# Kernel tuning notes

Hardware: AMD Instinct MI355X
Metric: run time of the kernel (lower is better)

Reference implementation:

```python
import jax, jax.numpy as jnp
import numpy as np


def setup_inputs() -> dict:
    key = jax.random.key(0)
    k1, k2 = jax.random.split(key)
    B, L1, L2, D = 8, 2048, 2048, 128
    seq_1 = jax.random.normal(k1, (B, L1, D), dtype=jnp.float32)
    seq_2 = jax.random.normal(k2, (B, L2, D), dtype=jnp.float32)
    return {"seq_1": seq_1, "seq_2": seq_2}


def reference(seq_1, seq_2):
    # e_ij: [B, L1, L2] cross-attention scores
    e_ij = jnp.einsum("bid,bjd->bij", seq_1, seq_2)
    # softmax over seq_2 positions (axis=2) to attend into seq_2
    w2 = jax.nn.softmax(e_ij, axis=2)
    # softmax over seq_1 positions (axis=1) to attend into seq_1
    w1 = jax.nn.softmax(e_ij, axis=1)
    seq_1_hat = jnp.einsum("bij,bjd->bid", w2, seq_2)  # [B, L1, D]
    seq_2_hat = jnp.einsum("bij,bid->bjd", w1, seq_1)  # [B, L2, D]
    return (seq_1_hat, seq_2_hat)
```

## Files before the change

kernel.cpp:

```cpp
#include <hip/hip_runtime.h>
#include <hip/hip_bf16.h>
#include <math.h>


#define LSEQ 2048
#define DIM  128
#define NBATCH 8
#define BM 128
#define BJ 128
#define NJT (LSEQ / BJ)
#define THR_DEFER 8.0f
#define PLANE (NBATCH * LSEQ * DIM)

typedef _Float16 halfT;
typedef halfT v8h  __attribute__((ext_vector_type(8)));
typedef float v16f __attribute__((ext_vector_type(16)));

__device__ __forceinline__ unsigned pk2u(float a, float b) {
    auto p = __builtin_amdgcn_cvt_pkrtz(a, b);
    return __builtin_bit_cast(unsigned, p);
}

__device__ __forceinline__ void gload16(const void* g, void* l) {
    __builtin_amdgcn_global_load_lds(
        (const __attribute__((address_space(1))) unsigned int*)g,
        (__attribute__((address_space(3))) unsigned int*)l, 16, 0, 0);
}

__device__ __forceinline__ v16f vz16() {
    v16f z;
    #pragma unroll
    for (int r = 0; r < 16; ++r) z[r] = 0.f;
    return z;
}

__global__ __launch_bounds__(256, 4)
void prepass_kernel(const float* __restrict__ S1, const float* __restrict__ S2,
                    short* __restrict__ ws)
{
    __shared__ short Th[DIM][66];
    const int lt = blockIdx.x;
    const int bb = blockIdx.y;
    const int tn = blockIdx.z;
    const float* src = (tn ? S2 : S1) + ((size_t)bb * LSEQ + (size_t)lt * 64) * DIM;
    short* hi = ws + (size_t)tn * 2 * PLANE + ((size_t)bb * LSEQ + (size_t)lt * 64) * DIM;
    short* tr = ws + (size_t)tn * 2 * PLANE + (size_t)PLANE
              + (size_t)bb * DIM * LSEQ + (size_t)lt * 64;
    const int tid = threadIdx.x;
    #pragma unroll
    for (int it = 0; it < 8; ++it) {
        int idx = tid + it * 256;
        int r = idx >> 5;
        int c = (idx & 31) * 4;
        float4 v = *(const float4*)(src + (size_t)r * DIM + c);
        halfT h0 = (halfT)v.x, h1 = (halfT)v.y, h2 = (halfT)v.z, h3 = (halfT)v.w;
        short b0 = __builtin_bit_cast(short, h0), b1 = __builtin_bit_cast(short, h1);
        short b2 = __builtin_bit_cast(short, h2), b3 = __builtin_bit_cast(short, h3);
        *(short4*)&hi[(size_t)r * DIM + c] = make_short4(b0, b1, b2, b3);
        Th[c + 0][r] = b0; Th[c + 1][r] = b1;
        Th[c + 2][r] = b2; Th[c + 3][r] = b3;
    }
    __syncthreads();
    #pragma unroll
    for (int it = 0; it < 16; ++it) {
        int idx = tid + it * 256;
        int d = idx >> 5;
        int c = (idx & 31) * 2;
        unsigned val = (unsigned)(unsigned short)Th[d][c]
                     | ((unsigned)(unsigned short)Th[d][c + 1] << 16);
        *(unsigned*)(tr + (size_t)d * LSEQ + c) = val;
    }
}

__global__ __launch_bounds__(1024, 1)
void xattn_main(const short* __restrict__ ws, float* __restrict__ out)
{
    __shared__ char pool[131072];
    __shared__ float maxp[4][4][32];
    __shared__ float sEx[4][4][32];

    const int tid  = threadIdx.x;
    const int lane = tid & 63;
    const int wave = tid >> 6;
    const int wA   = wave & 3;
    const int wB   = wave >> 2;
    const int li   = lane & 31;
    const int h    = lane >> 5;
    const int sl   = (li & 15) << 4;

    const int bx   = blockIdx.x;
    const int xcd  = bx & 7;
    const int slot = bx >> 3;
    const int g    = xcd * 2 + (slot >> 4);
    const int rt   = slot & 15;
    const int side = g >> 3;
    const int bb   = g & 7;

    const short* XHg = ws + (size_t)side * 2 * PLANE + ((size_t)bb * LSEQ + (size_t)rt * BM) * DIM;
    const short* YHg = ws + (size_t)(side ^ 1) * 2 * PLANE + (size_t)bb * LSEQ * DIM;
    const short* YTg = ws + (size_t)(side ^ 1) * 2 * PLANE + (size_t)PLANE + (size_t)bb * DIM * LSEQ;
    float* O = out + (size_t)side * PLANE + ((size_t)bb * LSEQ + (size_t)rt * BM) * DIM;

    v8h xv[8];
    {
        const short* xr = XHg + (size_t)(wA * 32 + li) * DIM + h * 8;
        #pragma unroll
        for (int ks = 0; ks < 8; ++ks)
            xv[ks] = *(const v8h*)(const void*)(xr + ks * 16);
    }

    float runm = -INFINITY, runs = 0.f;
    v16f o = vz16();

    const int ch0 = wave * 2;
    const int sr0 = ch0 * 4 + (lane >> 4);
    const int sr1 = (ch0 + 1) * 4 + (lane >> 4);
    const int sc0 = ((lane & 15) * 16) ^ ((sr0 & 15) << 4);
    const int sc1 = ((lane & 15) * 16) ^ ((sr1 & 15) << 4);

    auto STAGE_Y = [&](int jt) {
        gload16((const char*)YHg + ((size_t)(jt * BJ + sr0)) * 256 + sc0,
                pool + ch0 * 1024);
        gload16((const char*)YHg + ((size_t)(jt * BJ + sr1)) * 256 + sc1,
                pool + (ch0 + 1) * 1024);
    };
    auto STAGE_V = [&](int jt, int b) {
        gload16((const char*)YTg + (size_t)sr0 * (LSEQ * 2) + (size_t)jt * (BJ * 2) + sc0,
                pool + 32768 + b * 32768 + ch0 * 1024);
        gload16((const char*)YTg + (size_t)sr1 * (LSEQ * 2) + (size_t)jt * (BJ * 2) + sc1,
                pool + 32768 + b * 32768 + (ch0 + 1) * 1024);
    };

    STAGE_Y(0);
    STAGE_V(0, 0);
    asm volatile("s_waitcnt vmcnt(0)" ::: "memory");
    __syncthreads();

    const int yrow = wB * 32 + li;
    const int prow = wA * 32 + li;
    const int vrow = wB * 32 + li;
    char* PtB = pool + 98304;

    for (int jt = 0; jt < NJT; ++jt) {
        const int cur = jt & 1;

        v16f e = vz16();
        __builtin_amdgcn_s_setprio(1);
        #pragma unroll
        for (int ks = 0; ks < 8; ++ks) {
            v8h ya = *(const v8h*)(pool + yrow * 256 + ((ks * 32 + h * 16) ^ sl));
            e = __builtin_amdgcn_mfma_f32_32x32x16_f16(ya, xv[ks], e, 0, 0, 0);
        }
        __builtin_amdgcn_s_setprio(0);

        float a0 = fmaxf(fmaxf(e[0], e[1]),  fmaxf(e[2], e[3]));
        float a1 = fmaxf(fmaxf(e[4], e[5]),  fmaxf(e[6], e[7]));
        float a2 = fmaxf(fmaxf(e[8], e[9]),  fmaxf(e[10], e[11]));
        float a3 = fmaxf(fmaxf(e[12], e[13]), fmaxf(e[14], e[15]));
        float mt = fmaxf(fmaxf(a0, a1), fmaxf(a2, a3));
        mt = fmaxf(mt, __shfl_xor(mt, 32));
        if (lane < 32) maxp[wA][wB][lane] = mt;

        asm volatile("s_waitcnt lgkmcnt(0)" ::: "memory");
        __builtin_amdgcn_s_barrier();
        __builtin_amdgcn_sched_barrier(0);

        if (jt + 1 < NJT) {
            STAGE_Y(jt + 1);
            STAGE_V(jt + 1, cur ^ 1);
        }

        float m4 = fmaxf(fmaxf(maxp[wA][0][li], maxp[wA][1][li]),
                         fmaxf(maxp[wA][2][li], maxp[wA][3][li]));
        float f = 1.0f;
        if (m4 > runm + THR_DEFER) { f = __expf(runm - m4); runs *= f; runm = m4; }

        float s = 0.f;
        #pragma unroll
        for (int r = 0; r < 16; ++r) { e[r] = __expf(e[r] - runm); s += e[r]; }
        s += __shfl_xor(s, 32);
        runs += s;

        if (__any(f != 1.0f)) {
            #pragma unroll
            for (int r = 0; r < 16; ++r)
                o[r] *= __shfl(f, (r & 3) + 8 * (r >> 2) + 4 * h);
        }

        #pragma unroll
        for (int gq = 0; gq < 4; ++gq) {
            unsigned u0 = pk2u(e[gq * 4 + 0], e[gq * 4 + 1]);
            unsigned u1 = pk2u(e[gq * 4 + 2], e[gq * 4 + 3]);
            unsigned long long uu = (unsigned long long)u0 | ((unsigned long long)u1 << 32);
            const int gran = (wB * 4 + gq) ^ (li & 15);
            *(unsigned long long*)(PtB + prow * 256 + gran * 16 + h * 8) = uu;
        }

        asm volatile("s_waitcnt lgkmcnt(0)" ::: "memory");
        __builtin_amdgcn_s_barrier();
        __builtin_amdgcn_sched_barrier(0);

        const char* Vc = pool + 32768 + cur * 32768;
        __builtin_amdgcn_s_setprio(1);
        #pragma unroll
        for (int ks = 0; ks < 8; ++ks) {
            v8h pa = *(const v8h*)(PtB + prow * 256 + (((ks * 2 + h) ^ (li & 15)) << 4));
            v8h vb = *(const v8h*)(Vc + vrow * 256 + ((ks * 32 + h * 16) ^ sl));
            o = __builtin_amdgcn_mfma_f32_32x32x16_f16(pa, vb, o, 0, 0, 0);
        }
        __builtin_amdgcn_s_setprio(0);

        asm volatile("s_waitcnt vmcnt(0) lgkmcnt(0)" ::: "memory");
        __builtin_amdgcn_s_barrier();
        __builtin_amdgcn_sched_barrier(0);
    }

    if (lane < 32) sEx[wA][wB][lane] = runs;
    __syncthreads();
    const float inv = 1.0f / ((sEx[wA][0][li] + sEx[wA][1][li]) +
                              (sEx[wA][2][li] + sEx[wA][3][li]));
    #pragma unroll
    for (int r = 0; r < 16; ++r) {
        const int i = (r & 3) + 8 * (r >> 2) + 4 * h;
        const float fr = __shfl(inv, i);
        O[(size_t)(wA * 32 + i) * DIM + wB * 32 + li] = o[r] * fr;
    }
}

extern "C" void kernel_launch(void* const* d_in, const int* in_sizes, int n_in,
                              void* d_out, int out_size, void* d_ws, size_t ws_size,
                              hipStream_t stream) {
    const float* s1 = (const float*)d_in[0];
    const float* s2 = (const float*)d_in[1];
    float* out = (float*)d_out;
    short* ws = (short*)d_ws;
    prepass_kernel<<<dim3(LSEQ / 64, NBATCH, 2), 256, 0, stream>>>(s1, s2, ws);
    xattn_main<<<dim3(256), 1024, 0, stream>>>(ws, out);
}
```

Baseline: 68.81 us.

## Switch PV matmul to bf16, use a lagged row max, and restage Y/V buffers

The transposed value plane is now stored in bf16, and the probabilities are packed with v_cvt_pk_bf16_f32 so the PV MFMA runs in bf16. This widens the exponent range for the unnormalized weights. The softmax max now uses the previous tile's cross-wave maximum, which removes one block barrier per tile, and the rescale threshold drops to 4. Y is now double-buffered while V is single-buffered and staged after the PV step. Half of the X fragment is reloaded from global memory each tile to cut register pressure. The trade-offs are extra global loads, a risk of overflow from the lagged maximum, and serialization of the V load.

```diff
diff --git a/kernel.cpp b/kernel.cpp
--- a/kernel.cpp
+++ b/kernel.cpp
@@ -9,16 +9,24 @@
 #define BM 128
 #define BJ 128
 #define NJT (LSEQ / BJ)
-#define THR_DEFER 8.0f
+#define THR_DEFER 4.0f
 #define PLANE (NBATCH * LSEQ * DIM)
 
 typedef _Float16 halfT;
 typedef halfT v8h  __attribute__((ext_vector_type(8)));
+typedef short v8s  __attribute__((ext_vector_type(8)));
 typedef float v16f __attribute__((ext_vector_type(16)));
 
-__device__ __forceinline__ unsigned pk2u(float a, float b) {
-    auto p = __builtin_amdgcn_cvt_pkrtz(a, b);
-    return __builtin_bit_cast(unsigned, p);
+__device__ __forceinline__ unsigned pk2bf(float a, float b) {
+    unsigned r;
+    asm("v_cvt_pk_bf16_f32 %0, %1, %2" : "=v"(r) : "v"(a), "v"(b));
+    return r;
+}
+
+__device__ __forceinline__ short f2bf(float f) {
+    union { float f; unsigned u; } v; v.f = f;
+    unsigned r = (v.u + 0x7FFFu + ((v.u >> 16) & 1u)) >> 16;
+    return (short)r;
 }
 
 __device__ __forceinline__ void gload16(const void* g, void* l) {
@@ -54,11 +62,11 @@
         int c = (idx & 31) * 4;
         float4 v = *(const float4*)(src + (size_t)r * DIM + c);
         halfT h0 = (halfT)v.x, h1 = (halfT)v.y, h2 = (halfT)v.z, h3 = (halfT)v.w;
-        short b0 = __builtin_bit_cast(short, h0), b1 = __builtin_bit_cast(short, h1);
-        short b2 = __builtin_bit_cast(short, h2), b3 = __builtin_bit_cast(short, h3);
-        *(short4*)&hi[(size_t)r * DIM + c] = make_short4(b0, b1, b2, b3);
-        Th[c + 0][r] = b0; Th[c + 1][r] = b1;
-        Th[c + 2][r] = b2; Th[c + 3][r] = b3;
+        *(short4*)&hi[(size_t)r * DIM + c] = make_short4(
+            __builtin_bit_cast(short, h0), __builtin_bit_cast(short, h1),
+            __builtin_bit_cast(short, h2), __builtin_bit_cast(short, h3));
+        Th[c + 0][r] = f2bf(v.x); Th[c + 1][r] = f2bf(v.y);
+        Th[c + 2][r] = f2bf(v.z); Th[c + 3][r] = f2bf(v.w);
     }
     __syncthreads();
     #pragma unroll
@@ -76,7 +84,7 @@
 void xattn_main(const short* __restrict__ ws, float* __restrict__ out)
 {
     __shared__ char pool[131072];
-    __shared__ float maxp[4][4][32];
+    __shared__ float maxp[2][4][4][32];
     __shared__ float sEx[4][4][32];
 
     const int tid  = threadIdx.x;
@@ -101,15 +109,13 @@
     const short* YTg = ws + (size_t)(side ^ 1) * 2 * PLANE + (size_t)PLANE + (size_t)bb * DIM * LSEQ;
     float* O = out + (size_t)side * PLANE + ((size_t)bb * LSEQ + (size_t)rt * BM) * DIM;
 
-    v8h xv[8];
-    {
-        const short* xr = XHg + (size_t)(wA * 32 + li) * DIM + h * 8;
-        #pragma unroll
-        for (int ks = 0; ks < 8; ++ks)
-            xv[ks] = *(const v8h*)(const void*)(xr + ks * 16);
-    }
-
-    float runm = -INFINITY, runs = 0.f;
+    const short* xr = XHg + (size_t)(wA * 32 + li) * DIM + h * 8;
+    v8h xv[4];
+    #pragma unroll
+    for (int ks = 0; ks < 4; ++ks)
+        xv[ks] = *(const v8h*)(const void*)(xr + ks * 16);
+
+    float M = 0.f, runs = 0.f;
     v16f o = vz16();
 
     const int ch0 = wave * 2;
@@ -118,21 +124,21 @@
     const int sc0 = ((lane & 15) * 16) ^ ((sr0 & 15) << 4);
     const int sc1 = ((lane & 15) * 16) ^ ((sr1 & 15) << 4);
 
-    auto STAGE_Y = [&](int jt) {
+    auto STAGE_Y = [&](int jt, int b) {
         gload16((const char*)YHg + ((size_t)(jt * BJ + sr0)) * 256 + sc0,
-                pool + ch0 * 1024);
+                pool + b * 32768 + ch0 * 1024);
         gload16((const char*)YHg + ((size_t)(jt * BJ + sr1)) * 256 + sc1,
-                pool + (ch0 + 1) * 1024);
+                pool + b * 32768 + (ch0 + 1) * 1024);
     };
-    auto STAGE_V = [&](int jt, int b) {
+    auto STAGE_V = [&](int jt) {
         gload16((const char*)YTg + (size_t)sr0 * (LSEQ * 2) + (size_t)jt * (BJ * 2) + sc0,
-                pool + 32768 + b * 32768 + ch0 * 1024);
+                pool + 65536 + ch0 * 1024);
         gload16((const char*)YTg + (size_t)sr1 * (LSEQ * 2) + (size_t)jt * (BJ * 2) + sc1,
-                pool + 32768 + b * 32768 + (ch0 + 1) * 1024);
+                pool + 65536 + (ch0 + 1) * 1024);
     };
 
-    STAGE_Y(0);
-    STAGE_V(0, 0);
+    STAGE_Y(0, 0);
+    STAGE_V(0);
     asm volatile("s_waitcnt vmcnt(0)" ::: "memory");
     __syncthreads();
 
@@ -140,16 +146,28 @@
     const int prow = wA * 32 + li;
     const int vrow = wB * 32 + li;
     char* PtB = pool + 98304;
+    const char* Vc = pool + 65536;
 
     for (int jt = 0; jt < NJT; ++jt) {
         const int cur = jt & 1;
+        const char* Yc = pool + cur * 32768;
+
+        v8h xt[4];
+        #pragma unroll
+        for (int ks = 0; ks < 4; ++ks)
+            xt[ks] = *(const v8h*)(const void*)(xr + 64 + ks * 16);
 
         v16f e = vz16();
         __builtin_amdgcn_s_setprio(1);
         #pragma unroll
-        for (int ks = 0; ks < 8; ++ks) {
-            v8h ya = *(const v8h*)(pool + yrow * 256 + ((ks * 32 + h * 16) ^ sl));
+        for (int ks = 0; ks < 4; ++ks) {
+            v8h ya = *(const v8h*)(Yc + yrow * 256 + ((ks * 32 + h * 16) ^ sl));
             e = __builtin_amdgcn_mfma_f32_32x32x16_f16(ya, xv[ks], e, 0, 0, 0);
+        }
+        #pragma unroll
+        for (int ks = 4; ks < 8; ++ks) {
+            v8h ya = *(const v8h*)(Yc + yrow * 256 + ((ks * 32 + h * 16) ^ sl));
+            e = __builtin_amdgcn_mfma_f32_32x32x16_f16(ya, xt[ks - 4], e, 0, 0, 0);
         }
         __builtin_amdgcn_s_setprio(0);
 
@@ -159,25 +177,25 @@
         float a3 = fmaxf(fmaxf(e[12], e[13]), fmaxf(e[14], e[15]));
         float mt = fmaxf(fmaxf(a0, a1), fmaxf(a2, a3));
         mt = fmaxf(mt, __shfl_xor(mt, 32));
-        if (lane < 32) maxp[wA][wB][lane] = mt;
-
-        asm volatile("s_waitcnt lgkmcnt(0)" ::: "memory");
-        __builtin_amdgcn_s_barrier();
-        __builtin_amdgcn_sched_barrier(0);
-
-        if (jt + 1 < NJT) {
-            STAGE_Y(jt + 1);
-            STAGE_V(jt + 1, cur ^ 1);
-        }
-
-        float m4 = fmaxf(fmaxf(maxp[wA][0][li], maxp[wA][1][li]),
-                         fmaxf(maxp[wA][2][li], maxp[wA][3][li]));
+        if (lane < 32) maxp[cur][wA][wB][lane] = mt;
+
+        if (jt == 0) {
+            asm volatile("s_waitcnt lgkmcnt(0)" ::: "memory");
+            __builtin_amdgcn_s_barrier();
+        }
+        const int rb = (jt == 0) ? 0 : ((jt - 1) & 1);
+        float m4 = fmaxf(fmaxf(maxp[rb][wA][0][li], maxp[rb][wA][1][li]),
+                         fmaxf(maxp[rb][wA][2][li], maxp[rb][wA][3][li]));
         float f = 1.0f;
-        if (m4 > runm + THR_DEFER) { f = __expf(runm - m4); runs *= f; runm = m4; }
+        if (jt == 0) M = m4;
+        else if (m4 > M + THR_DEFER) { f = __expf(M - m4); M = m4; runs *= f; }
 
         float s = 0.f;
         #pragma unroll
-        for (int r = 0; r < 16; ++r) { e[r] = __expf(e[r] - runm); s += e[r]; }
+        for (int r = 0; r < 16; ++r) {
+            e[r] = __expf(e[r] - M);
+            s += e[r];
+        }
         s += __shfl_xor(s, 32);
         runs += s;
 
@@ -189,30 +207,35 @@
 
         #pragma unroll
         for (int gq = 0; gq < 4; ++gq) {
-            unsigned u0 = pk2u(e[gq * 4 + 0], e[gq * 4 + 1]);
-            unsigned u1 = pk2u(e[gq * 4 + 2], e[gq * 4 + 3]);
+            unsigned u0 = pk2bf(e[gq * 4 + 0], e[gq * 4 + 1]);
+            unsigned u1 = pk2bf(e[gq * 4 + 2], e[gq * 4 + 3]);
             unsigned long long uu = (unsigned long long)u0 | ((unsigned long long)u1 << 32);
             const int gran = (wB * 4 + gq) ^ (li & 15);
             *(unsigned long long*)(PtB + prow * 256 + gran * 16 + h * 8) = uu;
         }
 
+        asm volatile("s_waitcnt vmcnt(0)" ::: "memory");
         asm volatile("s_waitcnt lgkmcnt(0)" ::: "memory");
         __builtin_amdgcn_s_barrier();
         __builtin_amdgcn_sched_barrier(0);
 
-        const char* Vc = pool + 32768 + cur * 32768;
+        if (jt + 1 < NJT) STAGE_Y(jt + 1, cur ^ 1);
+
         __builtin_amdgcn_s_setprio(1);
         #pragma unroll
         for (int ks = 0; ks < 8; ++ks) {
-            v8h pa = *(const v8h*)(PtB + prow * 256 + (((ks * 2 + h) ^ (li & 15)) << 4));
-            v8h vb = *(const v8h*)(Vc + vrow * 256 + ((ks * 32 + h * 16) ^ sl));
-            o = __builtin_amdgcn_mfma_f32_32x32x16_f16(pa, vb, o, 0, 0, 0);
+            v8s pa = *(const v8s*)(PtB + prow * 256 + (((ks * 2 + h) ^ (li & 15)) << 4));
+            v8s vb = *(const v8s*)(Vc + vrow * 256 + ((ks * 32 + h * 16) ^ sl));
+            o = __builtin_amdgcn_mfma_f32_32x32x16_bf16(pa, vb, o, 0, 0, 0);
         }
         __builtin_amdgcn_s_setprio(0);
 
-        asm volatile("s_waitcnt vmcnt(0) lgkmcnt(0)" ::: "memory");
+        asm volatile("s_waitcnt vmcnt(0)" ::: "memory");
+        asm volatile("s_waitcnt lgkmcnt(0)" ::: "memory");
         __builtin_amdgcn_s_barrier();
         __builtin_amdgcn_sched_barrier(0);
+
+        if (jt + 1 < NJT) STAGE_V(jt + 1);
     }
 
     if (lane < 32) sEx[wA][wB][lane] = runs;
```

After: 80.11 us. +16.4%, slower.
